# Kernel tuning notes

Hardware: AMD Instinct MI355X
Metric: run time of the kernel (lower is better)

The kernel has to match this reference:

```python
import jax, jax.numpy as jnp
import numpy as np


def setup_inputs() -> dict:
    key = jax.random.key(0)
    k1, k2 = jax.random.split(key)
    N, S, C, H, W = 64, 16, 3, 128, 128
    inputs = jax.random.normal(k1, (N, C, H, W), dtype=jnp.float32)
    samples = jax.random.normal(k2, (N, S, C, H, W), dtype=jnp.float32)
    return {"inputs": inputs, "samples": samples}


def reference(inputs, samples):
    # diff: [N, S, C, H, W] via broadcast of inputs over the sample axis
    diff = samples - inputs[:, None]
    # squared distance per (batch, sample): sum over C, H, W -> [N, S]
    batch_loss = jnp.sum(diff * diff, axis=(2, 3, 4))
    # min over samples, then sum over batch -> scalar
    return jnp.sum(jnp.min(batch_loss, axis=1))
```

## Files before the change

### kernel.cpp

```cpp
#include <hip/hip_runtime.h>

constexpr int N_BATCH = 64;
constexpr int S_SAMP  = 16;
constexpr int CHW     = 3 * 128 * 128;
constexpr int CHW4    = CHW / 4;

__global__ __launch_bounds__(256) void pair_sqdist_kernel(
    const float* __restrict__ inputs,
    const float* __restrict__ samples,
    float* __restrict__ ws)
{
    const int b = blockIdx.x;
    const int n = b >> 4;
    const float4* __restrict__ inp = reinterpret_cast<const float4*>(inputs + (size_t)n * CHW);
    const float4* __restrict__ smp = reinterpret_cast<const float4*>(samples + (size_t)b * CHW);

    const int t = threadIdx.x;
    float acc = 0.0f;
    #pragma unroll 4
    for (int i = t; i < CHW4; i += 256) {
        float4 a = inp[i];
        float4 c = smp[i];
        float dx = c.x - a.x;
        float dy = c.y - a.y;
        float dz = c.z - a.z;
        float dw = c.w - a.w;
        acc += dx * dx + dy * dy + dz * dz + dw * dw;
    }

    #pragma unroll
    for (int off = 32; off > 0; off >>= 1)
        acc += __shfl_down(acc, off, 64);

    __shared__ float wave_part[4];
    const int wave = t >> 6;
    if ((t & 63) == 0) wave_part[wave] = acc;
    __syncthreads();
    if (t == 0) {
        ws[b] = wave_part[0] + wave_part[1] + wave_part[2] + wave_part[3];
    }
}

__global__ __launch_bounds__(64) void min_sum_kernel(
    const float* __restrict__ ws,
    float* __restrict__ out)
{
    const int n = threadIdx.x;
    const float* p = ws + n * S_SAMP;
    float m = p[0];
    #pragma unroll
    for (int s = 1; s < S_SAMP; ++s)
        m = fminf(m, p[s]);
    #pragma unroll
    for (int off = 32; off > 0; off >>= 1)
        m += __shfl_down(m, off, 64);
    if (n == 0) out[0] = m;
}

extern "C" void kernel_launch(void* const* d_in, const int* in_sizes, int n_in,
                              void* d_out, int out_size, void* d_ws, size_t ws_size,
                              hipStream_t stream) {
    const float* inputs  = (const float*)d_in[0];
    const float* samples = (const float*)d_in[1];
    float* out = (float*)d_out;
    float* ws  = (float*)d_ws;

    pair_sqdist_kernel<<<N_BATCH * S_SAMP, 256, 0, stream>>>(inputs, samples, ws);
    min_sum_kernel<<<1, 64, 0, stream>>>(ws, out);
}
```

Before: 283.7 us.

## Chunk spatial dimension and reuse input tile across all samples per block

Each block now handles one spatial chunk of one batch item across all 16 samples, loading the input chunk once into registers and streaming sample data with nontemporal loads. A second kernel sums chunk partials per pair, then takes the min over samples and the sum over the batch. This aims to cut redundant input reads and raise memory-level parallelism via many independent loads per thread. It adds register pressure from 16 accumulators and more per-block shuffle reductions.

```diff
diff --git a/kernel.cpp b/kernel.cpp
--- a/kernel.cpp
+++ b/kernel.cpp
@@ -3,58 +3,92 @@
 constexpr int N_BATCH = 64;
 constexpr int S_SAMP  = 16;
 constexpr int CHW     = 3 * 128 * 128;
-constexpr int CHW4    = CHW / 4;
+constexpr int NCHUNK  = 16;
+constexpr int CHUNK   = CHW / NCHUNK;
+constexpr int CHUNK4  = CHUNK / 4;
 
-__global__ __launch_bounds__(256) void pair_sqdist_kernel(
+typedef float v4f __attribute__((ext_vector_type(4)));
+
+__device__ __forceinline__ float sqdiff4(v4f s, v4f p) {
+    v4f d = s - p;
+    return d.x * d.x + d.y * d.y + d.z * d.z + d.w * d.w;
+}
+
+__global__ __launch_bounds__(256) void chunk_sqdist_kernel(
     const float* __restrict__ inputs,
     const float* __restrict__ samples,
     float* __restrict__ ws)
 {
     const int b = blockIdx.x;
     const int n = b >> 4;
-    const float4* __restrict__ inp = reinterpret_cast<const float4*>(inputs + (size_t)n * CHW);
-    const float4* __restrict__ smp = reinterpret_cast<const float4*>(samples + (size_t)b * CHW);
+    const int c = b & 15;
+    const int t = threadIdx.x;
 
-    const int t = threadIdx.x;
-    float acc = 0.0f;
-    #pragma unroll 4
-    for (int i = t; i < CHW4; i += 256) {
-        float4 a = inp[i];
-        float4 c = smp[i];
-        float dx = c.x - a.x;
-        float dy = c.y - a.y;
-        float dz = c.z - a.z;
-        float dw = c.w - a.w;
-        acc += dx * dx + dy * dy + dz * dz + dw * dw;
+    const v4f* __restrict__ inp =
+        reinterpret_cast<const v4f*>(inputs + (size_t)n * CHW + (size_t)c * CHUNK);
+    const v4f p0 = inp[t];
+    const v4f p1 = inp[t + 256];
+    const v4f p2 = inp[t + 512];
+
+    const float* __restrict__ smp_base =
+        samples + (size_t)n * S_SAMP * CHW + (size_t)c * CHUNK;
+
+    float acc[S_SAMP];
+    #pragma unroll
+    for (int s = 0; s < S_SAMP; ++s) {
+        const v4f* __restrict__ sp =
+            reinterpret_cast<const v4f*>(smp_base + (size_t)s * CHW);
+        v4f x0 = __builtin_nontemporal_load(sp + t);
+        v4f x1 = __builtin_nontemporal_load(sp + t + 256);
+        v4f x2 = __builtin_nontemporal_load(sp + t + 512);
+        acc[s] = sqdiff4(x0, p0) + sqdiff4(x1, p1) + sqdiff4(x2, p2);
     }
 
+    __shared__ float wave_part[4][S_SAMP];
+    const int wave = t >> 6;
     #pragma unroll
-    for (int off = 32; off > 0; off >>= 1)
-        acc += __shfl_down(acc, off, 64);
-
-    __shared__ float wave_part[4];
-    const int wave = t >> 6;
-    if ((t & 63) == 0) wave_part[wave] = acc;
+    for (int s = 0; s < S_SAMP; ++s) {
+        float a = acc[s];
+        #pragma unroll
+        for (int off = 32; off > 0; off >>= 1)
+            a += __shfl_down(a, off, 64);
+        if ((t & 63) == 0) wave_part[wave][s] = a;
+    }
     __syncthreads();
-    if (t == 0) {
-        ws[b] = wave_part[0] + wave_part[1] + wave_part[2] + wave_part[3];
+    if (t < S_SAMP) {
+        ws[(size_t)b * S_SAMP + t] =
+            wave_part[0][t] + wave_part[1][t] + wave_part[2][t] + wave_part[3][t];
     }
 }
 
-__global__ __launch_bounds__(64) void min_sum_kernel(
+__global__ __launch_bounds__(256) void reduce_kernel(
     const float* __restrict__ ws,
     float* __restrict__ out)
 {
-    const int n = threadIdx.x;
-    const float* p = ws + n * S_SAMP;
-    float m = p[0];
-    #pragma unroll
-    for (int s = 1; s < S_SAMP; ++s)
-        m = fminf(m, p[s]);
-    #pragma unroll
-    for (int off = 32; off > 0; off >>= 1)
-        m += __shfl_down(m, off, 64);
-    if (n == 0) out[0] = m;
+    __shared__ float pair[N_BATCH * S_SAMP];
+    const int t = threadIdx.x;
+    for (int p = t; p < N_BATCH * S_SAMP; p += 256) {
+        const int n = p >> 4;
+        const int s = p & 15;
+        const float* base = ws + (size_t)n * NCHUNK * S_SAMP + s;
+        float a = 0.0f;
+        #pragma unroll
+        for (int c = 0; c < NCHUNK; ++c)
+            a += base[(size_t)c * S_SAMP];
+        pair[p] = a;
+    }
+    __syncthreads();
+    if (t < N_BATCH) {
+        const float* pl = pair + t * S_SAMP;
+        float m = pl[0];
+        #pragma unroll
+        for (int s = 1; s < S_SAMP; ++s)
+            m = fminf(m, pl[s]);
+        #pragma unroll
+        for (int off = 32; off > 0; off >>= 1)
+            m += __shfl_down(m, off, 64);
+        if (t == 0) out[0] = m;
+    }
 }
 
 extern "C" void kernel_launch(void* const* d_in, const int* in_sizes, int n_in,
@@ -65,6 +99,6 @@
     float* out = (float*)d_out;
     float* ws  = (float*)d_ws;
 
-    pair_sqdist_kernel<<<N_BATCH * S_SAMP, 256, 0, stream>>>(inputs, samples, ws);
-    min_sum_kernel<<<1, 64, 0, stream>>>(ws, out);
+    chunk_sqdist_kernel<<<N_BATCH * NCHUNK, 256, 0, stream>>>(inputs, samples, ws);
+    reduce_kernel<<<1, 256, 0, stream>>>(ws, out);
 }
```

After: 268.6 us. -5.3%, faster.
